# Kernel tuning notes

Measured on AMD Instinct MI355X. Metric: run time of the kernel, lower is better.

The kernel has to match this reference:

```python
import jax, jax.numpy as jnp
import numpy as np

C = 512
NUM_HEADS = 4
GROUPS = 32
EPS = 1e-5


def setup_inputs() -> dict:
    key = jax.random.key(0)
    ks = jax.random.split(key, 7)
    x = jax.random.normal(ks[0], (1, C, 4, 32, 32), dtype=jnp.float32)
    norm_w = jax.random.normal(ks[1], (C,), dtype=jnp.float32) * 0.02 + 1.0
    norm_b = jax.random.normal(ks[2], (C,), dtype=jnp.float32) * 0.02
    # 1x1x1 Conv3d == pointwise linear over channels
    qkv_w = jax.random.normal(ks[3], (3 * C, C), dtype=jnp.float32) * (C ** -0.5)
    qkv_b = jax.random.normal(ks[4], (3 * C,), dtype=jnp.float32) * 0.02
    proj_w = jax.random.normal(ks[5], (C, C), dtype=jnp.float32) * (C ** -0.5)
    proj_b = jax.random.normal(ks[6], (C,), dtype=jnp.float32) * 0.02
    return {"x": x, "norm_w": norm_w, "norm_b": norm_b,
            "qkv_w": qkv_w, "qkv_b": qkv_b,
            "proj_w": proj_w, "proj_b": proj_b}


def reference(x, norm_w, norm_b, qkv_w, qkv_b, proj_w, proj_b):
    B, Cc, T, H, W = x.shape
    N = T * H * W
    nh = NUM_HEADS
    d = Cc // nh
    # GroupNorm(32, C), biased variance, eps=1e-5
    xg = x.reshape(B, GROUPS, Cc // GROUPS, N)
    mu = xg.mean(axis=(2, 3), keepdims=True)
    var = xg.var(axis=(2, 3), keepdims=True)
    h = ((xg - mu) * jax.lax.rsqrt(var + EPS)).reshape(B, Cc, N)
    h = h * norm_w[None, :, None] + norm_b[None, :, None]
    # QKV 1x1 conv as channel matmul: (B, 3C, N)
    qkv = jnp.einsum('oc,bcn->bon', qkv_w, h) + qkv_b[None, :, None]
    qkv = qkv.reshape(B, 3, nh, d, N)
    q, k, v = qkv[:, 0], qkv[:, 1], qkv[:, 2]  # each (B, nh, d, N)
    scale = d ** -0.5
    attn = jax.nn.softmax(jnp.einsum('bhdn,bhdm->bhnm', q, k) * scale, axis=-1)
    out = jnp.einsum('bhnm,bhdm->bhdn', attn, v).reshape(B, Cc, N)
    out = jnp.einsum('oc,bcn->bon', proj_w, out) + proj_b[None, :, None]
    return x + out.reshape(B, Cc, T, H, W)
```

## Files before the change

### kernel.cpp

```cpp
#include <hip/hip_runtime.h>
#include <hip/hip_bf16.h>

#define CDIM 512
#define NTOK 4096
#define NH 4
#define DH 128
#define NGRP 32
#define EPS 1e-5f
#define NSPLIT 4
#define KVBLK 64
#define TPS (NTOK/KVBLK/NSPLIT)

typedef __attribute__((ext_vector_type(8))) short bf16x8;
typedef __attribute__((ext_vector_type(4))) short short4v;
typedef __attribute__((ext_vector_type(4))) float f32x4;
typedef __attribute__((ext_vector_type(16))) float f32x16;
typedef __attribute__((ext_vector_type(2))) unsigned int u32x2;

__device__ inline unsigned short f2bf(float f){
  unsigned int u = __float_as_uint(f);
  u = (u + 0x7fffu + ((u >> 16) & 1u)) >> 16;
  return (unsigned short)u;
}

__device__ inline float bf2f(unsigned short u){
  return __uint_as_float(((unsigned int)u) << 16);
}

__device__ inline f32x4 mfma_bf16(bf16x8 a, bf16x8 b, f32x4 c){
  asm("v_mfma_f32_16x16x32_bf16 %0, %1, %2, %0" : "+v"(c) : "v"(a), "v"(b));
  return c;
}

__device__ inline f32x16 mfma32(bf16x8 a, bf16x8 b, f32x16 c){
  asm("v_mfma_f32_32x32x16_bf16 %0, %1, %2, %0" : "+v"(c) : "v"(a), "v"(b));
  return c;
}

__device__ inline unsigned int cvtpk(float lo, float hi){
  unsigned int r;
  asm("v_cvt_pk_bf16_f32 %0, %1, %2" : "=v"(r) : "v"(lo), "v"(hi));
  return r;
}

#define GLD16(gsrc, ldst) \
  __builtin_amdgcn_global_load_lds((__attribute__((address_space(1))) const void*)(gsrc), \
                                   (__attribute__((address_space(3))) void*)(ldst), 16, 0, 0)

#define KSC (0.088388347648318447f * 1.4426950408889634f)
#define INV_KSC (1.0f / KSC)
#define THR_RAW 60.0f
#define THR_K (THR_RAW * KSC)

__global__ __launch_bounds__(256) void k_convert(const float* __restrict__ qkv_w,
                                                 const float* __restrict__ proj_w,
                                                 unsigned short* __restrict__ qw,
                                                 unsigned short* __restrict__ pw){
  int stride = gridDim.x * blockDim.x;
  int i0 = blockIdx.x * blockDim.x + threadIdx.x;
  for (int i = i0; i < 3*CDIM*CDIM; i += stride) qw[i] = f2bf(qkv_w[i]);
  for (int i = i0; i < CDIM*CDIM; i += stride)   pw[i] = f2bf(proj_w[i]);
}

__global__ __launch_bounds__(256) void k_gnstats(const float* __restrict__ x,
                                                 float* __restrict__ stats){
  const int g = blockIdx.x, t = threadIdx.x;
  const f32x4* p = (const f32x4*)(x + (size_t)g * (16*NTOK));
  float s = 0.f, ss = 0.f;
  for (int i = t; i < 16*NTOK/4; i += 256){
    f32x4 v = p[i];
    s  += v[0]+v[1]+v[2]+v[3];
    ss += v[0]*v[0]+v[1]*v[1]+v[2]*v[2]+v[3]*v[3];
  }
  for (int off = 32; off > 0; off >>= 1){ s += __shfl_down(s, off); ss += __shfl_down(ss, off); }
  __shared__ float rs[4], rss[4];
  if ((t & 63) == 0){ rs[t>>6] = s; rss[t>>6] = ss; }
  __syncthreads();
  if (t == 0){
    float S  = rs[0]+rs[1]+rs[2]+rs[3];
    float SS = rss[0]+rss[1]+rss[2]+rss[3];
    const float inv = 1.f / (float)(16*NTOK);
    float mu  = S * inv;
    float var = SS * inv - mu*mu;
    stats[g]        = mu;
    stats[NGRP + g] = rsqrtf(var + EPS);
  }
}

__global__ __launch_bounds__(256) void k_gnapply(const float* __restrict__ x,
                                                 const float* __restrict__ stats,
                                                 const float* __restrict__ nw,
                                                 const float* __restrict__ nbias,
                                                 unsigned short* __restrict__ h_t){
  __shared__ float tile[64][68];
  const int n0 = blockIdx.x * 64, c0 = blockIdx.y * 64;
  const int t = threadIdx.x;
  {
    const int cl = t >> 2;
    #pragma unroll
    for (int i = 0; i < 4; i++){
      const int f4 = (t & 3) + i*4;
      *(f32x4*)&tile[cl][f4*4] = *(const f32x4*)(x + (size_t)(c0+cl)*NTOK + n0 + f4*4);
    }
  }
  __syncthreads();
  const int nl = t >> 2, cb = (t & 3) * 16;
  unsigned short ov[16] __attribute__((aligned(8)));
  #pragma unroll
  for (int j = 0; j < 16; j++){
    const int c = c0 + cb + j;
    const int grp = c >> 4;
    const float val = (tile[cb+j][nl] - stats[grp]) * stats[NGRP+grp] * nw[c] + nbias[c];
    ov[j] = f2bf(val);
  }
  unsigned short* dst = h_t + (size_t)(n0+nl)*CDIM + c0 + cb;
  #pragma unroll
  for (int j = 0; j < 4; j++) *(short4v*)(dst + j*4) = *(const short4v*)(ov + j*4);
}

template<int MODE>
__global__ __launch_bounds__(256) void k_gemm(const unsigned short* __restrict__ A,
                                              const unsigned short* __restrict__ Bt,
                                              const float* __restrict__ bias,
                                              const float* __restrict__ xres,
                                              unsigned short* __restrict__ q_t,
                                              unsigned short* __restrict__ k_t,
                                              unsigned short* __restrict__ vbuf,
                                              float* __restrict__ out,
                                              int K)
{
  __shared__ unsigned short Asm[128*32];
  __shared__ unsigned short Bsm[128*32];
  const int m0 = blockIdx.y * 128, n0 = blockIdx.x * 128;
  const int t = threadIdx.x;
  const int lane = t & 63, w = t >> 6;
  const int lo = lane & 15, g = lane >> 4;
  const int wr = w >> 1, wc = w & 1;
  f32x4 acc[4][4];
  #pragma unroll
  for (int i=0;i<4;i++)
    #pragma unroll
    for (int j=0;j<4;j++) acc[i][j] = f32x4{0.f,0.f,0.f,0.f};

  const int row = t >> 2, cb8 = (t & 3) * 8;
  for (int k0 = 0; k0 < K; k0 += 32){
    __syncthreads();
    *(bf16x8*)(Asm + row*32 + cb8)      = *(const bf16x8*)(A  + (size_t)(m0+row)*K    + k0 + cb8);
    *(bf16x8*)(Asm + (row+64)*32 + cb8) = *(const bf16x8*)(A  + (size_t)(m0+row+64)*K + k0 + cb8);
    *(bf16x8*)(Bsm + row*32 + cb8)      = *(const bf16x8*)(Bt + (size_t)(n0+row)*K    + k0 + cb8);
    *(bf16x8*)(Bsm + (row+64)*32 + cb8) = *(const bf16x8*)(Bt + (size_t)(n0+row+64)*K + k0 + cb8);
    __syncthreads();
    bf16x8 af[4], bfr[4];
    #pragma unroll
    for (int i=0;i<4;i++) af[i]  = *(const bf16x8*)(Asm + (wr*64 + i*16 + lo)*32 + g*8);
    #pragma unroll
    for (int j=0;j<4;j++) bfr[j] = *(const bf16x8*)(Bsm + (wc*64 + j*16 + lo)*32 + g*8);
    #pragma unroll
    for (int i=0;i<4;i++)
      #pragma unroll
      for (int j=0;j<4;j++)
        acc[i][j] = mfma_bf16(af[i], bfr[j], acc[i][j]);
  }

  if constexpr (MODE == 0){
    const int sQ = m0 >> 9;
    const int hh = (m0 >> 7) & 3;
    #pragma unroll
    for (int i=0;i<4;i++){
      const int ddb = wr*64 + i*16 + g*4;
      const int ob  = m0 + ddb;
      float b[4];
      #pragma unroll
      for (int r=0;r<4;r++) b[r] = bias[ob + r];
      #pragma unroll
      for (int j=0;j<4;j++){
        const int n = n0 + wc*64 + j*16 + lo;
        if (sQ < 2){
          unsigned short pk[4] __attribute__((aligned(8)));
          #pragma unroll
          for (int r=0;r<4;r++) pk[r] = f2bf(acc[i][j][r] + b[r]);
          unsigned short* dst = (sQ == 0 ? q_t : k_t) + ((size_t)hh*NTOK + n)*DH + ddb;
          *(short4v*)dst = *(const short4v*)pk;
        } else {
          #pragma unroll
          for (int r=0;r<4;r++)
            vbuf[((size_t)hh*DH + ddb + r)*NTOK + n] = f2bf(acc[i][j][r] + b[r]);
        }
      }
    }
  } else {
    #pragma unroll
    for (int i=0;i<4;i++){
      const int ob = m0 + wr*64 + i*16 + g*4;
      float b[4];
      #pragma unroll
      for (int r=0;r<4;r++) b[r] = bias[ob + r];
      #pragma unroll
      for (int j=0;j<4;j++){
        const int n = n0 + wc*64 + j*16 + lo;
        #pragma unroll
        for (int r=0;r<4;r++){
          size_t idx = (size_t)(ob + r)*NTOK + n;
          out[idx] = acc[i][j][r] + b[r] + xres[idx];
        }
      }
    }
  }
}

__global__ __launch_bounds__(512, 2) void k_attn(const unsigned short* __restrict__ q_t,
                                                 const unsigned short* __restrict__ k_t,
                                                 const unsigned short* __restrict__ vbuf,
                                                 unsigned short* __restrict__ opart,
                                                 float* __restrict__ mlbuf){
  const int h = blockIdx.y;
  const int qt = blockIdx.x >> 2, split = blockIdx.x & 3;
  const int t = threadIdx.x, w = t >> 6, lane = t & 63;
  const int la = lane & 31, hi = lane >> 5;
  const int s15 = la & 15, s7 = la & 7;
  const int nbq = qt * 256 + w * 32;

  __shared__ __align__(16) unsigned short Ksm[2][64*128];
  __shared__ __align__(16) unsigned short Vsm[2][128*64];
  __shared__ __align__(16) unsigned short Pt[8][32][76];

  const unsigned short* kg = k_t  + (size_t)h*NTOK*DH;
  const unsigned short* vg = vbuf + (size_t)h*DH*NTOK;

  auto stage = [&](int mt, int buf){
    const unsigned short* kgm = kg + (size_t)mt*KVBLK*DH;
    const unsigned short* vgm = vg + mt*KVBLK;
    #pragma unroll
    for (int rnd = 0; rnd < 2; rnd++){
      const int c = rnd*512 + t;
      const int row = c >> 4, col = c & 15;
      GLD16(kgm + (size_t)row*DH + ((col ^ (row & 15))*8), &Ksm[buf][c*8]);
    }
    #pragma unroll
    for (int rnd = 0; rnd < 2; rnd++){
      const int c = rnd*512 + t;
      const int row = c >> 3, col = c & 7;
      GLD16(vgm + (size_t)row*NTOK + ((col ^ (row & 7))*8), &Vsm[buf][c*8]);
    }
  };

  bf16x8 qa[8];
  {
    const unsigned short* qr = q_t + ((size_t)h*NTOK + nbq + la)*DH + hi*8;
    #pragma unroll
    for (int ks=0;ks<8;ks++) qa[ks] = *(const bf16x8*)(qr + ks*16);
  }

  float mk = -1e30f;
  float lsum = 0.f;
  f32x16 oacc[4];
  #pragma unroll
  for (int dt=0;dt<4;dt++)
    #pragma unroll
    for (int r=0;r<16;r++) oacc[dt][r] = 0.f;

  const int mt0 = split * TPS;
  stage(mt0, 0);
  int cur = 0;
  for (int it = 0; it < TPS; it++){
    __syncthreads();
    if (it + 1 < TPS) stage(mt0 + it + 1, cur ^ 1);

    const unsigned short* Ks = Ksm[cur];
    const unsigned short* Vs = Vsm[cur];
    unsigned short* Pw = &Pt[w][0][0];

    #pragma unroll
    for (int half = 0; half < 2; half++){
      f32x16 s;
      #pragma unroll
      for (int r=0;r<16;r++) s[r] = 0.f;
      #pragma unroll
      for (int ks=0; ks<8; ks++){
        bf16x8 kf = *(const bf16x8*)(Ks + (half*32 + la)*128 + (((2*ks + hi) ^ s15) * 8));
        s = mfma32(kf, qa[ks], s);
      }
      float hmax = s[0];
      #pragma unroll
      for (int r=1;r<16;r++) hmax = fmaxf(hmax, s[r]);
      hmax = fmaxf(hmax, __shfl_xor(hmax, 32));
      const float hk = hmax * KSC;
      if (!__all(hk <= mk + THR_K)){
        const float mnk = fmaxf(mk, hk);
        const float al  = exp2f(mk - mnk);
        mk = mnk;
        lsum *= al;
        #pragma unroll
        for (int dt=0;dt<4;dt++)
          #pragma unroll
          for (int r=0;r<16;r++) oacc[dt][r] *= al;
      }
      #pragma unroll
      for (int r=0;r<16;r++){
        s[r] = exp2f(fmaf(s[r], KSC, -mk));
        lsum += s[r];
      }
      #pragma unroll
      for (int g2=0; g2<4; g2++){
        u32x2 pk;
        pk[0] = cvtpk(s[4*g2+0], s[4*g2+1]);
        pk[1] = cvtpk(s[4*g2+2], s[4*g2+3]);
        *(u32x2*)(Pw + la*76 + half*32 + 8*g2 + 4*hi) = pk;
      }
      __builtin_amdgcn_wave_barrier();
      #pragma unroll
      for (int kst2=0; kst2<2; kst2++){
        const int kst = half*2 + kst2;
        bf16x8 pb = *(const bf16x8*)(Pw + la*76 + kst*16 + hi*8);
        #pragma unroll
        for (int dt=0; dt<4; dt++){
          bf16x8 vf = *(const bf16x8*)(Vs + (dt*32 + la)*64 + (((2*kst + hi) ^ s7) * 8));
          oacc[dt] = mfma32(vf, pb, oacc[dt]);
        }
      }
    }
    cur ^= 1;
  }
  const float lt = lsum + __shfl_xor(lsum, 32);
  const float linv = 1.f / lt;
  unsigned short* Od = opart + ((size_t)(split*NH + h)*NTOK + nbq + la)*DH;
  #pragma unroll
  for (int dt=0;dt<4;dt++)
    #pragma unroll
    for (int g2=0; g2<4; g2++){
      unsigned short pk[4] __attribute__((aligned(8)));
      #pragma unroll
      for (int j=0;j<4;j++) pk[j] = f2bf(oacc[dt][4*g2+j] * linv);
      *(short4v*)(Od + dt*32 + 8*g2 + 4*hi) = *(const short4v*)pk;
    }
  if (hi == 0){
    float* ml = mlbuf + ((size_t)(split*NH + h)*NTOK + nbq)*2;
    ml[la*2]     = mk * INV_KSC;
    ml[la*2 + 1] = lt;
  }
}

__global__ __launch_bounds__(256) void k_merge(const unsigned short* __restrict__ opart,
                                               const float* __restrict__ mlbuf,
                                               unsigned short* __restrict__ ao_t){
  const int h = blockIdx.y;
  const int n = blockIdx.x*2 + (threadIdx.x >> 7);
  const int d = threadIdx.x & 127;
  float ms[NSPLIT], ls[NSPLIT], m = -1e30f;
  #pragma unroll
  for (int s=0;s<NSPLIT;s++){
    const float* ml = mlbuf + ((size_t)(s*NH + h)*NTOK + n)*2;
    ms[s] = ml[0]; ls[s] = ml[1];
    m = fmaxf(m, ms[s]);
  }
  float wsum = 0.f, o = 0.f;
  #pragma unroll
  for (int s=0;s<NSPLIT;s++){
    float wgt = exp2f((ms[s]-m)*KSC) * ls[s];
    wsum += wgt;
    o += wgt * bf2f(opart[((size_t)(s*NH + h)*NTOK + n)*DH + d]);
  }
  ao_t[(size_t)n*CDIM + h*DH + d] = f2bf(o / wsum);
}

extern "C" void kernel_launch(void* const* d_in, const int* in_sizes, int n_in,
                              void* d_out, int out_size, void* d_ws, size_t ws_size,
                              hipStream_t stream){
  const float* x      = (const float*)d_in[0];
  const float* norm_w = (const float*)d_in[1];
  const float* norm_b = (const float*)d_in[2];
  const float* qkv_w  = (const float*)d_in[3];
  const float* qkv_b  = (const float*)d_in[4];
  const float* proj_w = (const float*)d_in[5];
  const float* proj_b = (const float*)d_in[6];
  float* out = (float*)d_out;

  char* ws = (char*)d_ws;
  unsigned short* qw  = (unsigned short*)(ws);
  unsigned short* pw  = (unsigned short*)(ws + 1572864);
  unsigned short* h_t = (unsigned short*)(ws + 2097152);
  unsigned short* q_t = (unsigned short*)(ws + 6291456);
  unsigned short* k_t = (unsigned short*)(ws + 10485760);
  unsigned short* vb  = (unsigned short*)(ws + 14680064);
  unsigned short* ao  = (unsigned short*)(ws + 18874368);
  float* stats        = (float*)(ws + 23068672);
  unsigned short* opart = (unsigned short*)(ws + 23072768);
  float* mlbuf        = (float*)(ws + 39849984);

  hipLaunchKernelGGL(k_convert, dim3(1024), dim3(256), 0, stream, qkv_w, proj_w, qw, pw);
  hipLaunchKernelGGL(k_gnstats, dim3(32), dim3(256), 0, stream, x, stats);
  hipLaunchKernelGGL(k_gnapply, dim3(64, 8), dim3(256), 0, stream, x, stats, norm_w, norm_b, h_t);
  hipLaunchKernelGGL((k_gemm<0>), dim3(32, 12), dim3(256), 0, stream,
                     qw, h_t, qkv_b, (const float*)nullptr,
                     q_t, k_t, vb, (float*)nullptr, 512);
  hipLaunchKernelGGL(k_attn, dim3(16*NSPLIT, NH), dim3(512), 0, stream, q_t, k_t, vb, opart, mlbuf);
  hipLaunchKernelGGL(k_merge, dim3(NTOK/2, NH), dim3(256), 0, stream, opart, mlbuf, ao);
  hipLaunchKernelGGL((k_gemm<1>), dim3(32, 4), dim3(256), 0, stream,
                     pw, ao, proj_b, x,
                     (unsigned short*)nullptr, (unsigned short*)nullptr, (unsigned short*)nullptr, out, 512);
}
```

Before: 127.5 us.

## Single-buffer attention K/V tiles, raise occupancy, and use 8-way KV split

The attention kernel drops its double-buffered K/V shared-memory staging in favour of a single buffer with a sync before and after each load. This cuts LDS use so the launch bound can ask for 4 blocks per CU instead of 2. When the workspace is large enough, the KV sequence is split 8 ways instead of 4, doubling the grid to fill more CUs, and the merge kernel is templated on the split count. The cost is that the copy/compute overlap is lost, there is an extra barrier per tile, and the merge kernel reads twice as many partial outputs.

```diff
diff --git a/kernel.cpp b/kernel.cpp
--- a/kernel.cpp
+++ b/kernel.cpp
@@ -7,9 +7,7 @@
 #define DH 128
 #define NGRP 32
 #define EPS 1e-5f
-#define NSPLIT 4
 #define KVBLK 64
-#define TPS (NTOK/KVBLK/NSPLIT)
 
 typedef __attribute__((ext_vector_type(8))) short bf16x8;
 typedef __attribute__((ext_vector_type(4))) short short4v;
@@ -208,39 +206,41 @@
   }
 }
 
-__global__ __launch_bounds__(512, 2) void k_attn(const unsigned short* __restrict__ q_t,
+template<int NS>
+__global__ __launch_bounds__(512, 4) void k_attn(const unsigned short* __restrict__ q_t,
                                                  const unsigned short* __restrict__ k_t,
                                                  const unsigned short* __restrict__ vbuf,
                                                  unsigned short* __restrict__ opart,
                                                  float* __restrict__ mlbuf){
+  const int TPS = NTOK/KVBLK/NS;
   const int h = blockIdx.y;
-  const int qt = blockIdx.x >> 2, split = blockIdx.x & 3;
+  const int qt = blockIdx.x / NS, split = blockIdx.x % NS;
   const int t = threadIdx.x, w = t >> 6, lane = t & 63;
   const int la = lane & 31, hi = lane >> 5;
   const int s15 = la & 15, s7 = la & 7;
   const int nbq = qt * 256 + w * 32;
 
-  __shared__ __align__(16) unsigned short Ksm[2][64*128];
-  __shared__ __align__(16) unsigned short Vsm[2][128*64];
+  __shared__ __align__(16) unsigned short Ksm[64*128];
+  __shared__ __align__(16) unsigned short Vsm[128*64];
   __shared__ __align__(16) unsigned short Pt[8][32][76];
 
   const unsigned short* kg = k_t  + (size_t)h*NTOK*DH;
   const unsigned short* vg = vbuf + (size_t)h*DH*NTOK;
 
-  auto stage = [&](int mt, int buf){
+  auto stage = [&](int mt){
     const unsigned short* kgm = kg + (size_t)mt*KVBLK*DH;
     const unsigned short* vgm = vg + mt*KVBLK;
     #pragma unroll
     for (int rnd = 0; rnd < 2; rnd++){
       const int c = rnd*512 + t;
       const int row = c >> 4, col = c & 15;
-      GLD16(kgm + (size_t)row*DH + ((col ^ (row & 15))*8), &Ksm[buf][c*8]);
+      GLD16(kgm + (size_t)row*DH + ((col ^ (row & 15))*8), &Ksm[c*8]);
     }
     #pragma unroll
     for (int rnd = 0; rnd < 2; rnd++){
       const int c = rnd*512 + t;
       const int row = c >> 3, col = c & 7;
-      GLD16(vgm + (size_t)row*NTOK + ((col ^ (row & 7))*8), &Vsm[buf][c*8]);
+      GLD16(vgm + (size_t)row*NTOK + ((col ^ (row & 7))*8), &Vsm[c*8]);
     }
   };
 
@@ -260,14 +260,13 @@
     for (int r=0;r<16;r++) oacc[dt][r] = 0.f;
 
   const int mt0 = split * TPS;
-  stage(mt0, 0);
-  int cur = 0;
   for (int it = 0; it < TPS; it++){
     __syncthreads();
-    if (it + 1 < TPS) stage(mt0 + it + 1, cur ^ 1);
-
-    const unsigned short* Ks = Ksm[cur];
-    const unsigned short* Vs = Vsm[cur];
+    stage(mt0 + it);
+    __syncthreads();
+
+    const unsigned short* Ks = Ksm;
+    const unsigned short* Vs = Vsm;
     unsigned short* Pw = &Pt[w][0][0];
 
     #pragma unroll
@@ -319,7 +318,6 @@
         }
       }
     }
-    cur ^= 1;
   }
   const float lt = lsum + __shfl_xor(lsum, 32);
   const float linv = 1.f / lt;
@@ -340,22 +338,23 @@
   }
 }
 
+template<int NS>
 __global__ __launch_bounds__(256) void k_merge(const unsigned short* __restrict__ opart,
                                                const float* __restrict__ mlbuf,
                                                unsigned short* __restrict__ ao_t){
   const int h = blockIdx.y;
   const int n = blockIdx.x*2 + (threadIdx.x >> 7);
   const int d = threadIdx.x & 127;
-  float ms[NSPLIT], ls[NSPLIT], m = -1e30f;
-  #pragma unroll
-  for (int s=0;s<NSPLIT;s++){
+  float ms[NS], ls[NS], m = -1e30f;
+  #pragma unroll
+  for (int s=0;s<NS;s++){
     const float* ml = mlbuf + ((size_t)(s*NH + h)*NTOK + n)*2;
     ms[s] = ml[0]; ls[s] = ml[1];
     m = fmaxf(m, ms[s]);
   }
   float wsum = 0.f, o = 0.f;
   #pragma unroll
-  for (int s=0;s<NSPLIT;s++){
+  for (int s=0;s<NS;s++){
     float wgt = exp2f((ms[s]-m)*KSC) * ls[s];
     wsum += wgt;
     o += wgt * bf2f(opart[((size_t)(s*NH + h)*NTOK + n)*DH + d]);
@@ -385,7 +384,6 @@
   unsigned short* ao  = (unsigned short*)(ws + 18874368);
   float* stats        = (float*)(ws + 23068672);
   unsigned short* opart = (unsigned short*)(ws + 23072768);
-  float* mlbuf        = (float*)(ws + 39849984);
 
   hipLaunchKernelGGL(k_convert, dim3(1024), dim3(256), 0, stream, qkv_w, proj_w, qw, pw);
   hipLaunchKernelGGL(k_gnstats, dim3(32), dim3(256), 0, stream, x, stats);
@@ -393,8 +391,21 @@
   hipLaunchKernelGGL((k_gemm<0>), dim3(32, 12), dim3(256), 0, stream,
                      qw, h_t, qkv_b, (const float*)nullptr,
                      q_t, k_t, vb, (float*)nullptr, 512);
-  hipLaunchKernelGGL(k_attn, dim3(16*NSPLIT, NH), dim3(512), 0, stream, q_t, k_t, vb, opart, mlbuf);
-  hipLaunchKernelGGL(k_merge, dim3(NTOK/2, NH), dim3(256), 0, stream, opart, mlbuf, ao);
+
+  if (ws_size >= 57675776ULL){
+    constexpr int NS = 8;
+    float* mlbuf = (float*)(ws + 23072768 + (size_t)NS*NH*NTOK*DH*2);
+    hipLaunchKernelGGL((k_attn<NS>), dim3((NTOK/256)*NS, NH), dim3(512), 0, stream,
+                       q_t, k_t, vb, opart, mlbuf);
+    hipLaunchKernelGGL((k_merge<NS>), dim3(NTOK/2, NH), dim3(256), 0, stream, opart, mlbuf, ao);
+  } else {
+    constexpr int NS = 4;
+    float* mlbuf = (float*)(ws + 23072768 + (size_t)NS*NH*NTOK*DH*2);
+    hipLaunchKernelGGL((k_attn<NS>), dim3((NTOK/256)*NS, NH), dim3(512), 0, stream,
+                       q_t, k_t, vb, opart, mlbuf);
+    hipLaunchKernelGGL((k_merge<NS>), dim3(NTOK/2, NH), dim3(256), 0, stream, opart, mlbuf, ao);
+  }
+
   hipLaunchKernelGGL((k_gemm<1>), dim3(32, 4), dim3(256), 0, stream,
                      pw, ao, proj_b, x,
                      (unsigned short*)nullptr, (unsigned short*)nullptr, (unsigned short*)nullptr, out, 512);
```

Result: slower. 210.1 us (+64.9%).
